# Performance work log

Hardware: AMD Instinct MI355X
Metric: run time of the kernel (lower is better)

Reference implementation:

```python
import jax, jax.numpy as jnp
import numpy as np

HIDDEN = 32
ODE_H = 0.1      # rk4 fixed step size (torchdiffeq options step_size=0.1)
ODE_STEPS = 10   # integrate t in [0, 1]


def gcn_conv(x, W, b, edge_index, n):
    """PyG GCNConv: symmetric norm with self-loops; x' = D^-1/2 (A+I) D^-1/2 (x W) + b."""
    h = x @ W                                  # [n, out]
    src, dst = edge_index[0], edge_index[1]
    deg = jnp.ones((n,), h.dtype).at[dst].add(1.0)   # +1 for self-loop
    dinv = jax.lax.rsqrt(deg)
    coef = (dinv[src] * dinv[dst])[:, None]
    agg = jnp.zeros_like(h).at[dst].add(h[src] * coef)
    agg = agg + h * (dinv * dinv)[:, None]     # self-loop term
    return agg + b


def ode_rk4(x0, edge_index, Wg, bg, wt, n):
    """RK4 integration of psi(t,x)=relu(GCN(x)) * sigmoid(t * wt) from t=0 to 1."""
    def f(t, x):
        gate = jax.nn.sigmoid(t * wt)          # [hidden], Linear(1,h,no bias).sigmoid()
        return jax.nn.relu(gcn_conv(x, Wg, bg, edge_index, n)) * gate

    h = ODE_H
    def step(x, t):
        k1 = f(t, x)
        k2 = f(t + h * 0.5, x + (h * 0.5) * k1)
        k3 = f(t + h * 0.5, x + (h * 0.5) * k2)
        k4 = f(t + h, x + h * k3)
        return x + (h / 6.0) * (k1 + 2.0 * k2 + 2.0 * k3 + k4), None

    ts = jnp.arange(ODE_STEPS, dtype=x0.dtype) * h
    xf, _ = jax.lax.scan(step, x0, ts)
    return xf


def setup_inputs() -> dict:
    key = jax.random.key(0)
    ks = jax.random.split(key, 16)
    N, IN, H = 100000, 128, HIDDEN
    E, DE = 1600000, 800000

    inp = {
        "H_t": jax.random.normal(ks[0], (N, IN), jnp.float32),
        "A_pos_t": jax.random.randint(ks[1], (2, E), 0, N),
        "A_neg_t": jax.random.randint(ks[2], (2, E), 0, N),
        "dA_pos": jax.random.randint(ks[3], (2, DE), 0, N),
        "dA_neg": jax.random.randint(ks[4], (2, DE), 0, N),
        # init GCN
        "W_init": jax.random.normal(ks[5], (IN, H), jnp.float32) / np.sqrt(IN),
        "b_init": jnp.zeros((H,), jnp.float32),
        # pos ODE func
        "W_pos": jax.random.normal(ks[6], (H, H), jnp.float32) / np.sqrt(H),
        "b_pos": jnp.zeros((H,), jnp.float32),
        "wt_pos": jax.random.normal(ks[7], (H,), jnp.float32),
        # neg ODE func
        "W_neg": jax.random.normal(ks[8], (H, H), jnp.float32) / np.sqrt(H),
        "b_neg": jnp.zeros((H,), jnp.float32),
        "wt_neg": jax.random.normal(ks[9], (H,), jnp.float32),
        # combine + layernorm
        "W_comb": jax.random.normal(ks[10], (2 * H, H), jnp.float32) / np.sqrt(2 * H),
        "b_comb": jnp.zeros((H,), jnp.float32),
        "ln_g": jnp.ones((H,), jnp.float32),
        "ln_b": jnp.zeros((H,), jnp.float32),
    }
    return inp


def reference(H_t, A_pos_t, A_neg_t, dA_pos, dA_neg,
              W_init, b_init, W_pos, b_pos, wt_pos,
              W_neg, b_neg, wt_neg, W_comb, b_comb, ln_g, ln_b):
    n = H_t.shape[0]
    edges_all = jnp.concatenate([A_pos_t, A_neg_t], axis=1)
    H = jax.nn.relu(gcn_conv(H_t, W_init, b_init, edges_all, n))   # [n, hidden]
    Z_pos = ode_rk4(H, dA_pos, W_pos, b_pos, wt_pos, n)
    Z_neg = ode_rk4(H, dA_neg, W_neg, b_neg, wt_neg, n)
    Z = jnp.concatenate([Z_pos, Z_neg], axis=-1) @ W_comb + b_comb # [n, hidden]
    mu = jnp.mean(Z, axis=-1, keepdims=True)
    var = jnp.var(Z, axis=-1, keepdims=True)
    return (Z - mu) * jax.lax.rsqrt(var + 1e-5) * ln_g + ln_b
```

## Files before the change

### kernel.cpp

```cpp
#include <hip/hip_runtime.h>
#include <math.h>


#define TPB 256
#define SCAN_T 1024

typedef _Float16 h8 __attribute__((ext_vector_type(8)));
typedef float f8 __attribute__((ext_vector_type(8)));


struct SegG { const int* src; const int* dst; int n; int goff; };
struct FSeg { const int* src; const int* dst; int n; const int* offs; int* cur; };

__global__ void count4(SegG s0, SegG s1, SegG s2, SegG s3, int* __restrict__ cnt3,
                       int* __restrict__ rank) {
    int i = blockIdx.x * blockDim.x + threadIdx.x;
    SegG s; int e;
    if (i < s0.n) { s = s0; e = i; }
    else if (i < s0.n + s1.n) { s = s1; e = i - s0.n; }
    else if (i < s0.n + s1.n + s2.n) { s = s2; e = i - s0.n - s1.n; }
    else if (i < s0.n + s1.n + s2.n + s3.n) { s = s3; e = i - s0.n - s1.n - s2.n; }
    else return;
    int r = atomicAdd(&cnt3[s.goff + s.dst[e]], 1);
    if (rank) rank[i] = r;
}

__global__ void fill4_rank(SegG s0, SegG s1, SegG s2, SegG s3,
                           const int* __restrict__ offs3, const int* __restrict__ rank,
                           int* __restrict__ csr) {
    int i = blockIdx.x * blockDim.x + threadIdx.x;
    SegG s; int e;
    if (i < s0.n) { s = s0; e = i; }
    else if (i < s0.n + s1.n) { s = s1; e = i - s0.n; }
    else if (i < s0.n + s1.n + s2.n) { s = s2; e = i - s0.n - s1.n; }
    else if (i < s0.n + s1.n + s2.n + s3.n) { s = s3; e = i - s0.n - s1.n - s2.n; }
    else return;
    csr[offs3[s.goff + s.dst[e]] + rank[i]] = s.src[e];
}

__global__ void fill4(FSeg s0, FSeg s1, FSeg s2, FSeg s3, int* __restrict__ csr) {
    int i = blockIdx.x * blockDim.x + threadIdx.x;
    FSeg s; int e;
    if (i < s0.n) { s = s0; e = i; }
    else if (i < s0.n + s1.n) { s = s1; e = i - s0.n; }
    else if (i < s0.n + s1.n + s2.n) { s = s2; e = i - s0.n - s1.n; }
    else if (i < s0.n + s1.n + s2.n + s3.n) { s = s3; e = i - s0.n - s1.n - s2.n; }
    else return;
    int d = s.dst[e];
    int pos = s.offs[d] + atomicAdd(&s.cur[d], 1);
    csr[pos] = s.src[e];
}

__global__ void dinv_from_cnt(const int* __restrict__ cnt, float* __restrict__ dinv, int n) {
    int i = blockIdx.x * blockDim.x + threadIdx.x;
    if (i < n) dinv[i] = rsqrtf(1.0f + (float)cnt[i]);
}

__global__ void scan_block(const int* __restrict__ in, int n, int* __restrict__ out,
                           int* __restrict__ bsums) {
    __shared__ int sh[SCAN_T];
    int tx = threadIdx.x;
    int g = blockIdx.x * SCAN_T + tx;
    int v = (g < n) ? in[g] : 0;
    sh[tx] = v;
    __syncthreads();
    for (int off = 1; off < SCAN_T; off <<= 1) {
        int t = (tx >= off) ? sh[tx - off] : 0;
        __syncthreads();
        sh[tx] += t;
        __syncthreads();
    }
    if (g < n) out[g] = sh[tx] - v;
    if (tx == SCAN_T - 1) bsums[blockIdx.x] = sh[tx];
}

__global__ void scan_sums(int* __restrict__ bsums, int nb) {
    __shared__ int sh[SCAN_T];
    int tx = threadIdx.x;
    int v = (tx < nb) ? bsums[tx] : 0;
    sh[tx] = v;
    __syncthreads();
    for (int off = 1; off < SCAN_T; off <<= 1) {
        int t = (tx >= off) ? sh[tx - off] : 0;
        __syncthreads();
        sh[tx] += t;
        __syncthreads();
    }
    if (tx < nb) bsums[tx] = sh[tx] - v;
}

__global__ void scan_add(int* __restrict__ offs, const int* __restrict__ bsums, int n, int total) {
    int g = blockIdx.x * blockDim.x + threadIdx.x;
    if (g < n) offs[g] += bsums[g >> 10];
    if (g == 0) offs[n] = total;
}


__global__ void mm32_kernel(const float* __restrict__ x, const float* __restrict__ W,
                            const float* __restrict__ dinv, _Float16* __restrict__ hs, int N) {
    __shared__ float Ws[32][32];
    __shared__ float xs[8][32];
    int tid = threadIdx.x;
    for (int i = tid; i < 32 * 32; i += TPB) Ws[i >> 5][i & 31] = W[i];
    int base = blockIdx.x * 8;
    {
        int idx = base * 32 + tid;
        xs[tid >> 5][tid & 31] = (idx < N * 32) ? x[idx] : 0.0f;
    }
    __syncthreads();
    int row = tid >> 5, c = tid & 31;
    int gr = base + row;
    float acc = 0.0f;
#pragma unroll
    for (int k = 0; k < 32; ++k) acc += xs[row][k] * Ws[k][c];
    if (gr < N) hs[gr * 32 + c] = (_Float16)(acc * dinv[gr]);
}

__global__ void mm128_kernel(const float* __restrict__ x, const float* __restrict__ W,
                             const float* __restrict__ dinv, _Float16* __restrict__ hs, int N) {
    __shared__ float Ws[128][32];
    __shared__ float xs[8][128];
    int tid = threadIdx.x;
    for (int i = tid; i < 128 * 32; i += TPB) Ws[i >> 5][i & 31] = W[i];
    int base = blockIdx.x * 8;
    for (int i = tid; i < 8 * 128; i += TPB) {
        int idx = base * 128 + i;
        xs[i >> 7][i & 127] = (idx < N * 128) ? x[idx] : 0.0f;
    }
    __syncthreads();
    int row = tid >> 5, c = tid & 31;
    int gr = base + row;
    float acc = 0.0f;
#pragma unroll
    for (int k = 0; k < 128; ++k) acc += xs[row][k] * Ws[k][c];
    if (gr < N) hs[gr * 32 + c] = (_Float16)(acc * dinv[gr]);
}


struct Job {
    const int* offs; const int* csr;
    const _Float16* hs_in; _Float16* hs_out;
    const float* dinv; const float* dinv_next;
    const float* bias; const float* wt;
    _Float16* ksum; float* x;
    const float* W;
};

__global__ __launch_bounds__(TPB) void agg_stage(Job jp, Job jn, int nbg, float t,
                                                 int stage, int do_mm, int split,
                                                 float* __restrict__ x2, int N) {
    __shared__ float Ws[32][32];
    __shared__ float xts[64][36];
    __shared__ int soffs[65];

    bool isP; int bid;
    if (split) {
        int xcd = blockIdx.x & 7;
        isP = xcd < 4;
        bid = ((int)blockIdx.x >> 3) * 4 + (xcd & 3);
        if (bid >= nbg) return;
    } else {
        isP = (int)blockIdx.x < nbg;
        bid = isP ? blockIdx.x : (blockIdx.x - nbg);
    }
    const Job& J = isP ? jp : jn;
    int nbase = bid * 64;
    int tid = threadIdx.x;
    int lnode = tid >> 2, q = tid & 3;
    int node = nbase + lnode;
    bool valid = node < N;

    if (do_mm) {
        for (int i = tid; i < 32 * 32; i += TPB) Ws[i >> 5][i & 31] = J.W[i];
    }
    if (tid < 65) {
        int ix = nbase + tid; if (ix > N) ix = N;
        soffs[tid] = J.offs[ix];
    }
    __syncthreads();

    f8 xrow;
#pragma unroll
    for (int j = 0; j < 8; ++j) xrow[j] = 0.f;

    if (valid) {
        const h8* hsv = (const h8*)J.hs_in;
        const int* __restrict__ csr = J.csr;
        int r0 = soffs[lnode], r1 = soffs[lnode + 1];
        f8 acc = __builtin_convertvector(hsv[node * 4 + q], f8);
        int i = r0;
        for (; i + 4 <= r1; i += 4) {
            int s0 = csr[i], s1 = csr[i + 1], s2 = csr[i + 2], s3 = csr[i + 3];
            h8 v0 = hsv[s0 * 4 + q];
            h8 v1 = hsv[s1 * 4 + q];
            h8 v2 = hsv[s2 * 4 + q];
            h8 v3 = hsv[s3 * 4 + q];
            acc += (__builtin_convertvector(v0, f8) + __builtin_convertvector(v1, f8))
                 + (__builtin_convertvector(v2, f8) + __builtin_convertvector(v3, f8));
        }
        for (; i < r1; ++i)
            acc += __builtin_convertvector(hsv[csr[i] * 4 + q], f8);

        float dv = J.dinv[node];
        f8 bb = ((const f8*)J.bias)[q];
        f8 kv;
#pragma unroll
        for (int j = 0; j < 8; ++j) kv[j] = fmaxf(acc[j] * dv + bb[j], 0.f);
        if (J.wt) {
            f8 w = ((const f8*)J.wt)[q];
#pragma unroll
            for (int j = 0; j < 8; ++j) kv[j] *= 1.f / (1.f + expf(-t * w[j]));
        }
        int idx = node * 4 + q;
        f8* x8 = (f8*)J.x;
        h8* ks8 = (h8*)J.ksum;
        if (stage == 0) {
            x8[idx] = kv;
            ((f8*)x2)[idx] = kv;
            xrow = kv;
        } else if (stage == 4) {
            f8 ks = __builtin_convertvector(ks8[idx], f8);
            f8 xv = x8[idx];
            const float cc = 0.1f / 6.0f;
#pragma unroll
            for (int j = 0; j < 8; ++j) xv[j] += cc * (ks[j] + kv[j]);
            x8[idx] = xv;
            xrow = xv;
        } else {
            float a = (stage == 3) ? 0.1f : 0.05f;
            f8 xv = x8[idx];
#pragma unroll
            for (int j = 0; j < 8; ++j) xrow[j] = xv[j] + a * kv[j];
            if (stage == 1) {
                ks8[idx] = __builtin_convertvector(kv, h8);
            } else {
                f8 ks = __builtin_convertvector(ks8[idx], f8);
#pragma unroll
                for (int j = 0; j < 8; ++j) ks[j] += 2.f * kv[j];
                ks8[idx] = __builtin_convertvector(ks, h8);
            }
        }
    }

    if (do_mm) {
        if (valid) {
#pragma unroll
            for (int j = 0; j < 8; ++j) xts[lnode][q * 8 + j] = xrow[j];
        }
        __syncthreads();
        if (valid) {
            f8 accm;
#pragma unroll
            for (int j = 0; j < 8; ++j) accm[j] = 0.f;
#pragma unroll
            for (int k = 0; k < 32; ++k) {
                float xv = xts[lnode][k];
                f8 w = *(const f8*)&Ws[k][q * 8];
                accm += xv * w;
            }
            accm *= J.dinv_next[node];
            ((h8*)J.hs_out)[node * 4 + q] = __builtin_convertvector(accm, h8);
        }
    }
}


__global__ void combine_kernel(const float* __restrict__ zp, const float* __restrict__ zn,
                               const float* __restrict__ Wc, const float* __restrict__ bc,
                               const float* __restrict__ g, const float* __restrict__ be,
                               float* __restrict__ out, int N) {
    __shared__ float Ws[64][32];
    __shared__ float zs[8][64];
    int tid = threadIdx.x;
    for (int i = tid; i < 64 * 32; i += TPB) Ws[i >> 5][i & 31] = Wc[i];
    int base = blockIdx.x * 8;
    {
        int r = tid >> 5, c = tid & 31;
        int gr = base + r;
        zs[r][c] = (gr < N) ? zp[gr * 32 + c] : 0.0f;
        zs[r][32 + c] = (gr < N) ? zn[gr * 32 + c] : 0.0f;
    }
    __syncthreads();
    int row = tid >> 5, c = tid & 31;
    int gr = base + row;
    float acc = bc[c];
#pragma unroll
    for (int k = 0; k < 64; ++k) acc += zs[row][k] * Ws[k][c];
    float s = acc, sq = acc * acc;
#pragma unroll
    for (int off = 16; off; off >>= 1) {
        s += __shfl_xor(s, off, 32);
        sq += __shfl_xor(sq, off, 32);
    }
    float mu = s * (1.0f / 32.0f);
    float var = sq * (1.0f / 32.0f) - mu * mu;
    float y = (acc - mu) * rsqrtf(var + 1e-5f) * g[c] + be[c];
    if (gr < N) out[gr * 32 + c] = y;
}


extern "C" void kernel_launch(void* const* d_in, const int* in_sizes, int n_in,
                              void* d_out, int out_size, void* d_ws, size_t ws_size,
                              hipStream_t stream) {
    const float* H_t = (const float*)d_in[0];
    const int* Apos = (const int*)d_in[1];
    const int* Aneg = (const int*)d_in[2];
    const int* dApos = (const int*)d_in[3];
    const int* dAneg = (const int*)d_in[4];
    const float* W_init = (const float*)d_in[5];
    const float* b_init = (const float*)d_in[6];
    const float* W_pos = (const float*)d_in[7];
    const float* b_pos = (const float*)d_in[8];
    const float* wt_pos = (const float*)d_in[9];
    const float* W_neg = (const float*)d_in[10];
    const float* b_neg = (const float*)d_in[11];
    const float* wt_neg = (const float*)d_in[12];
    const float* W_comb = (const float*)d_in[13];
    const float* b_comb = (const float*)d_in[14];
    const float* ln_g = (const float*)d_in[15];
    const float* ln_b = (const float*)d_in[16];

    const int N = in_sizes[0] / 128;
    const int E1 = in_sizes[1] / 2;
    const int E2 = in_sizes[2] / 2;
    const int DE1 = in_sizes[3] / 2;
    const int DE2 = in_sizes[4] / 2;
    const int Etot = E1 + E2 + DE1 + DE2;

    const int* Apos_src = Apos, * Apos_dst = Apos + E1;
    const int* Aneg_src = Aneg, * Aneg_dst = Aneg + E2;
    const int* dApos_src = dApos, * dApos_dst = dApos + DE1;
    const int* dAneg_src = dAneg, * dAneg_dst = dAneg + DE2;

    const size_t n32 = (size_t)N * 32;
    const size_t szf = n32 * 4;
    const size_t szh = n32 * 2;
    auto al = [](size_t b) { return (b + 255) & ~(size_t)255; };

    size_t small_bytes = 3 * al((size_t)(3 * N) * 4)
                       + al((3 * (size_t)N + 1) * 4)
                       + al((size_t)Etot * 4)
                       + al(SCAN_T * 4);
    size_t need_merged = 2 * al(szf) + 6 * al(szh) + small_bytes;
    size_t need_rank = need_merged + al((size_t)Etot * 4);
    bool merged = ws_size >= need_merged + 4096;
    bool use_rank = ws_size >= need_rank + 4096;

    char* p = (char*)d_ws;
    auto alloc = [&](size_t bytes) -> void* {
        void* r = (void*)p;
        p += al(bytes);
        return r;
    };
    float* x_pos = (float*)alloc(szf);
    float* x_neg = (float*)alloc(szf);
    _Float16* ksum_p = (_Float16*)alloc(szh);
    _Float16* ksum_n = merged ? (_Float16*)alloc(szh) : ksum_p;
    _Float16* hs_pa = (_Float16*)alloc(szh);
    _Float16* hs_pb = (_Float16*)alloc(szh);
    _Float16* hs_na = merged ? (_Float16*)alloc(szh) : hs_pa;
    _Float16* hs_nb = merged ? (_Float16*)alloc(szh) : hs_pb;
    float* dinv3 = (float*)alloc((size_t)(3 * N) * 4);
    int* cnt3 = (int*)alloc((size_t)(3 * N) * 4);
    int* cur3 = (int*)alloc((size_t)(3 * N) * 4);
    int* offs3 = (int*)alloc((3 * (size_t)N + 1) * 4);
    int* csr3 = (int*)alloc((size_t)Etot * 4);
    int* bsums = (int*)alloc(SCAN_T * 4);
    int* rank = use_rank ? (int*)alloc((size_t)Etot * 4) : nullptr;

    size_t used = (size_t)(p - (char*)d_ws);
    if (used > ws_size) used = ws_size;

    hipMemsetAsync(d_ws, 0, used, stream);

    float* dinv_all = dinv3, * dinv_pos = dinv3 + N, * dinv_neg = dinv3 + 2 * N;
    const int* offs_all = offs3, * offs_pos = offs3 + N, * offs_neg = offs3 + 2 * N;

    dim3 blk(TPB);
    auto gblk = [](int n) { return dim3((n + TPB - 1) / TPB); };
    dim3 grid_rows((N + 7) / 8);
    const int nb64 = (N + 63) / 64;
    const int n3 = 3 * N;
    const int nbs = (n3 + SCAN_T - 1) / SCAN_T;
    const int nsplit = ((nb64 + 3) / 4) * 8;

    SegG s0 = { Apos_src, Apos_dst, E1, 0 };
    SegG s1 = { Aneg_src, Aneg_dst, E2, 0 };
    SegG s2 = { dApos_src, dApos_dst, DE1, N };
    SegG s3 = { dAneg_src, dAneg_dst, DE2, 2 * N };
    count4<<<gblk(Etot), blk, 0, stream>>>(s0, s1, s2, s3, cnt3, rank);
    dinv_from_cnt<<<gblk(n3), blk, 0, stream>>>(cnt3, dinv3, n3);
    scan_block<<<nbs, SCAN_T, 0, stream>>>(cnt3, n3, offs3, bsums);
    scan_sums<<<1, SCAN_T, 0, stream>>>(bsums, nbs);
    scan_add<<<gblk(n3), blk, 0, stream>>>(offs3, bsums, n3, Etot);
    if (use_rank) {
        fill4_rank<<<gblk(Etot), blk, 0, stream>>>(s0, s1, s2, s3, offs3, rank, csr3);
    } else {
        FSeg f0 = { Apos_src, Apos_dst, E1, offs3, cur3 };
        FSeg f1 = { Aneg_src, Aneg_dst, E2, offs3, cur3 };
        FSeg f2 = { dApos_src, dApos_dst, DE1, offs3 + N, cur3 + N };
        FSeg f3 = { dAneg_src, dAneg_dst, DE2, offs3 + 2 * N, cur3 + 2 * N };
        fill4<<<gblk(Etot), blk, 0, stream>>>(f0, f1, f2, f3, csr3);
    }

    auto mkjob = [&](const int* offs, const _Float16* hs_in, _Float16* hs_out,
                     const float* dinv, const float* dinv_next, const float* bias,
                     const float* wt, _Float16* ksum, float* x, const float* W) {
        Job j; j.offs = offs; j.csr = csr3; j.hs_in = hs_in; j.hs_out = hs_out;
        j.dinv = dinv; j.dinv_next = dinv_next; j.bias = bias; j.wt = wt;
        j.ksum = ksum; j.x = x; j.W = W; return j;
    };

    mm128_kernel<<<grid_rows, blk, 0, stream>>>(H_t, W_init, dinv_all, hs_pa, N);
    {
        Job j0 = mkjob(offs_all, hs_pa, hs_pb, dinv_all, dinv_pos, b_init,
                       nullptr, nullptr, x_pos, W_pos);
        agg_stage<<<nb64, blk, 0, stream>>>(j0, j0, nb64, 0.0f, 0, 1, 0, x_neg, N);
    }

    if (merged) {
        mm32_kernel<<<grid_rows, blk, 0, stream>>>(x_neg, W_neg, dinv_neg, hs_nb, N);
        for (int s = 0; s < 10; ++s) {
            float t0 = 0.1f * (float)s;
            int last_mm = (s == 9) ? 0 : 1;
            Job p1 = mkjob(offs_pos, hs_pb, hs_pa, dinv_pos, dinv_pos, b_pos, wt_pos, ksum_p, x_pos, W_pos);
            Job n1 = mkjob(offs_neg, hs_nb, hs_na, dinv_neg, dinv_neg, b_neg, wt_neg, ksum_n, x_neg, W_neg);
            agg_stage<<<nsplit, blk, 0, stream>>>(p1, n1, nb64, t0, 1, 1, 1, nullptr, N);
            Job p2 = p1; p2.hs_in = hs_pa; p2.hs_out = hs_pb;
            Job n2 = n1; n2.hs_in = hs_na; n2.hs_out = hs_nb;
            agg_stage<<<nsplit, blk, 0, stream>>>(p2, n2, nb64, t0 + 0.05f, 2, 1, 1, nullptr, N);
            agg_stage<<<nsplit, blk, 0, stream>>>(p1, n1, nb64, t0 + 0.05f, 3, 1, 1, nullptr, N);
            agg_stage<<<nsplit, blk, 0, stream>>>(p2, n2, nb64, t0 + 0.1f, 4, last_mm, 1, nullptr, N);
        }
    } else {
        for (int ode = 0; ode < 2; ++ode) {
            float* x = ode ? x_neg : x_pos;
            const float* W = ode ? W_neg : W_pos;
            const float* b = ode ? b_neg : b_pos;
            const float* wt = ode ? wt_neg : wt_pos;
            const float* dinv = ode ? dinv_neg : dinv_pos;
            const int* offs = ode ? offs_neg : offs_pos;
            if (ode == 1) {
                mm32_kernel<<<grid_rows, blk, 0, stream>>>(x, W, dinv, hs_pb, N);
            }
            for (int s = 0; s < 10; ++s) {
                float t0 = 0.1f * (float)s;
                int last_mm = (s == 9) ? 0 : 1;
                Job j1 = mkjob(offs, hs_pb, hs_pa, dinv, dinv, b, wt, ksum_p, x, W);
                Job j2 = j1; j2.hs_in = hs_pa; j2.hs_out = hs_pb;
                agg_stage<<<nb64, blk, 0, stream>>>(j1, j1, nb64, t0, 1, 1, 0, nullptr, N);
                agg_stage<<<nb64, blk, 0, stream>>>(j2, j2, nb64, t0 + 0.05f, 2, 1, 0, nullptr, N);
                agg_stage<<<nb64, blk, 0, stream>>>(j1, j1, nb64, t0 + 0.05f, 3, 1, 0, nullptr, N);
                agg_stage<<<nb64, blk, 0, stream>>>(j2, j2, nb64, t0 + 0.1f, 4, last_mm, 0, nullptr, N);
            }
        }
    }

    combine_kernel<<<grid_rows, blk, 0, stream>>>(x_pos, x_neg, W_comb, b_comb, ln_g, ln_b,
                                                  (float*)d_out, N);
}
```

Baseline: 2.043 ms.

## Replicate CSR degree counters per XCD to localize histogram atomics

Keeps eight copies of the per-node degree counters, one per XCD, chosen by reading the hardware XCC_ID register. Each edge does its atomic increment on its own die's copy with workgroup scope, which avoids atomics bouncing across dies. A merge kernel sums the copies and computes dinv, and a fused scan pass turns them into per-XCD base offsets for the fill step. The cost is eight times the counter memory, extra merge traffic, and a reliance on workgroup-scope atomics staying coherent within an XCD's L2.

```diff
diff --git a/kernel.cpp b/kernel.cpp
--- a/kernel.cpp
+++ b/kernel.cpp
@@ -7,6 +7,12 @@
 
 typedef _Float16 h8 __attribute__((ext_vector_type(8)));
 typedef float f8 __attribute__((ext_vector_type(8)));
+
+__device__ __forceinline__ int xcc_id() {
+    unsigned v;
+    asm volatile("s_getreg_b32 %0, hwreg(HW_REG_XCC_ID, 0, 4)" : "=s"(v));
+    return (int)(v & 7u);
+}
 
 
 struct SegG { const int* src; const int* dst; int n; int goff; };
@@ -25,6 +31,32 @@
     if (rank) rank[i] = r;
 }
 
+__global__ void count4_xcd(SegG s0, SegG s1, SegG s2, SegG s3,
+                           int* __restrict__ rep, int n3, int* __restrict__ rank) {
+    int i = blockIdx.x * blockDim.x + threadIdx.x;
+    SegG s; int e;
+    if (i < s0.n) { s = s0; e = i; }
+    else if (i < s0.n + s1.n) { s = s1; e = i - s0.n; }
+    else if (i < s0.n + s1.n + s2.n) { s = s2; e = i - s0.n - s1.n; }
+    else if (i < s0.n + s1.n + s2.n + s3.n) { s = s3; e = i - s0.n - s1.n - s2.n; }
+    else return;
+    int xcd = xcc_id();
+    int r = __hip_atomic_fetch_add(&rep[xcd * n3 + s.goff + s.dst[e]], 1,
+                                   __ATOMIC_RELAXED, __HIP_MEMORY_SCOPE_WORKGROUP);
+    rank[i] = (xcd << 28) | r;
+}
+
+__global__ void merge_cnt(const int* __restrict__ rep, int n3,
+                          int* __restrict__ cnt, float* __restrict__ dinv) {
+    int i = blockIdx.x * blockDim.x + threadIdx.x;
+    if (i >= n3) return;
+    int c = 0;
+#pragma unroll
+    for (int x = 0; x < 8; ++x) c += rep[x * n3 + i];
+    cnt[i] = c;
+    dinv[i] = rsqrtf(1.0f + (float)c);
+}
+
 __global__ void fill4_rank(SegG s0, SegG s1, SegG s2, SegG s3,
                            const int* __restrict__ offs3, const int* __restrict__ rank,
                            int* __restrict__ csr) {
@@ -36,6 +68,22 @@
     else if (i < s0.n + s1.n + s2.n + s3.n) { s = s3; e = i - s0.n - s1.n - s2.n; }
     else return;
     csr[offs3[s.goff + s.dst[e]] + rank[i]] = s.src[e];
+}
+
+__global__ void fill4_rank_xcd(SegG s0, SegG s1, SegG s2, SegG s3,
+                               const int* __restrict__ rep, int n3,
+                               const int* __restrict__ rank, int* __restrict__ csr) {
+    int i = blockIdx.x * blockDim.x + threadIdx.x;
+    SegG s; int e;
+    if (i < s0.n) { s = s0; e = i; }
+    else if (i < s0.n + s1.n) { s = s1; e = i - s0.n; }
+    else if (i < s0.n + s1.n + s2.n) { s = s2; e = i - s0.n - s1.n; }
+    else if (i < s0.n + s1.n + s2.n + s3.n) { s = s3; e = i - s0.n - s1.n - s2.n; }
+    else return;
+    unsigned rv = (unsigned)rank[i];
+    int x = (int)(rv >> 28);
+    int lr = (int)(rv & 0x0FFFFFFFu);
+    csr[rep[x * n3 + s.goff + s.dst[e]] + lr] = s.src[e];
 }
 
 __global__ void fill4(FSeg s0, FSeg s1, FSeg s2, FSeg s3, int* __restrict__ csr) {
@@ -92,6 +140,23 @@
 __global__ void scan_add(int* __restrict__ offs, const int* __restrict__ bsums, int n, int total) {
     int g = blockIdx.x * blockDim.x + threadIdx.x;
     if (g < n) offs[g] += bsums[g >> 10];
+    if (g == 0) offs[n] = total;
+}
+
+__global__ void scan_add_fuse(int* __restrict__ offs, const int* __restrict__ bsums,
+                              int n, int total, int* __restrict__ rep) {
+    int g = blockIdx.x * blockDim.x + threadIdx.x;
+    if (g < n) {
+        int off = offs[g] + bsums[g >> 10];
+        offs[g] = off;
+        int run = off;
+#pragma unroll
+        for (int x = 0; x < 8; ++x) {
+            int t = rep[x * n + g];
+            rep[x * n + g] = run;
+            run += t;
+        }
+    }
     if (g == 0) offs[n] = total;
 }
 
@@ -326,6 +391,7 @@
     const int DE1 = in_sizes[3] / 2;
     const int DE2 = in_sizes[4] / 2;
     const int Etot = E1 + E2 + DE1 + DE2;
+    const int n3 = 3 * N;
 
     const int* Apos_src = Apos, * Apos_dst = Apos + E1;
     const int* Aneg_src = Aneg, * Aneg_dst = Aneg + E2;
@@ -337,14 +403,16 @@
     const size_t szh = n32 * 2;
     auto al = [](size_t b) { return (b + 255) & ~(size_t)255; };
 
-    size_t small_bytes = 3 * al((size_t)(3 * N) * 4)
-                       + al((3 * (size_t)N + 1) * 4)
+    size_t small_bytes = 3 * al((size_t)n3 * 4)
+                       + al(((size_t)n3 + 1) * 4)
                        + al((size_t)Etot * 4)
                        + al(SCAN_T * 4);
     size_t need_merged = 2 * al(szf) + 6 * al(szh) + small_bytes;
     size_t need_rank = need_merged + al((size_t)Etot * 4);
+    size_t need_xcd = need_rank + al((size_t)8 * n3 * 4);
     bool merged = ws_size >= need_merged + 4096;
     bool use_rank = ws_size >= need_rank + 4096;
+    bool use_xcd = ws_size >= need_xcd + 4096;
 
     char* p = (char*)d_ws;
     auto alloc = [&](size_t bytes) -> void* {
@@ -360,13 +428,14 @@
     _Float16* hs_pb = (_Float16*)alloc(szh);
     _Float16* hs_na = merged ? (_Float16*)alloc(szh) : hs_pa;
     _Float16* hs_nb = merged ? (_Float16*)alloc(szh) : hs_pb;
-    float* dinv3 = (float*)alloc((size_t)(3 * N) * 4);
-    int* cnt3 = (int*)alloc((size_t)(3 * N) * 4);
-    int* cur3 = (int*)alloc((size_t)(3 * N) * 4);
-    int* offs3 = (int*)alloc((3 * (size_t)N + 1) * 4);
+    float* dinv3 = (float*)alloc((size_t)n3 * 4);
+    int* cnt3 = (int*)alloc((size_t)n3 * 4);
+    int* cur3 = (int*)alloc((size_t)n3 * 4);
+    int* offs3 = (int*)alloc(((size_t)n3 + 1) * 4);
     int* csr3 = (int*)alloc((size_t)Etot * 4);
     int* bsums = (int*)alloc(SCAN_T * 4);
     int* rank = use_rank ? (int*)alloc((size_t)Etot * 4) : nullptr;
+    int* rep = use_xcd ? (int*)alloc((size_t)8 * n3 * 4) : nullptr;
 
     size_t used = (size_t)(p - (char*)d_ws);
     if (used > ws_size) used = ws_size;
@@ -380,7 +449,6 @@
     auto gblk = [](int n) { return dim3((n + TPB - 1) / TPB); };
     dim3 grid_rows((N + 7) / 8);
     const int nb64 = (N + 63) / 64;
-    const int n3 = 3 * N;
     const int nbs = (n3 + SCAN_T - 1) / SCAN_T;
     const int nsplit = ((nb64 + 3) / 4) * 8;
 
@@ -388,19 +456,28 @@
     SegG s1 = { Aneg_src, Aneg_dst, E2, 0 };
     SegG s2 = { dApos_src, dApos_dst, DE1, N };
     SegG s3 = { dAneg_src, dAneg_dst, DE2, 2 * N };
-    count4<<<gblk(Etot), blk, 0, stream>>>(s0, s1, s2, s3, cnt3, rank);
-    dinv_from_cnt<<<gblk(n3), blk, 0, stream>>>(cnt3, dinv3, n3);
-    scan_block<<<nbs, SCAN_T, 0, stream>>>(cnt3, n3, offs3, bsums);
-    scan_sums<<<1, SCAN_T, 0, stream>>>(bsums, nbs);
-    scan_add<<<gblk(n3), blk, 0, stream>>>(offs3, bsums, n3, Etot);
-    if (use_rank) {
-        fill4_rank<<<gblk(Etot), blk, 0, stream>>>(s0, s1, s2, s3, offs3, rank, csr3);
+    if (use_xcd) {
+        count4_xcd<<<gblk(Etot), blk, 0, stream>>>(s0, s1, s2, s3, rep, n3, rank);
+        merge_cnt<<<gblk(n3), blk, 0, stream>>>(rep, n3, cnt3, dinv3);
+        scan_block<<<nbs, SCAN_T, 0, stream>>>(cnt3, n3, offs3, bsums);
+        scan_sums<<<1, SCAN_T, 0, stream>>>(bsums, nbs);
+        scan_add_fuse<<<gblk(n3), blk, 0, stream>>>(offs3, bsums, n3, Etot, rep);
+        fill4_rank_xcd<<<gblk(Etot), blk, 0, stream>>>(s0, s1, s2, s3, rep, n3, rank, csr3);
     } else {
-        FSeg f0 = { Apos_src, Apos_dst, E1, offs3, cur3 };
-        FSeg f1 = { Aneg_src, Aneg_dst, E2, offs3, cur3 };
-        FSeg f2 = { dApos_src, dApos_dst, DE1, offs3 + N, cur3 + N };
-        FSeg f3 = { dAneg_src, dAneg_dst, DE2, offs3 + 2 * N, cur3 + 2 * N };
-        fill4<<<gblk(Etot), blk, 0, stream>>>(f0, f1, f2, f3, csr3);
+        count4<<<gblk(Etot), blk, 0, stream>>>(s0, s1, s2, s3, cnt3, rank);
+        dinv_from_cnt<<<gblk(n3), blk, 0, stream>>>(cnt3, dinv3, n3);
+        scan_block<<<nbs, SCAN_T, 0, stream>>>(cnt3, n3, offs3, bsums);
+        scan_sums<<<1, SCAN_T, 0, stream>>>(bsums, nbs);
+        scan_add<<<gblk(n3), blk, 0, stream>>>(offs3, bsums, n3, Etot);
+        if (use_rank) {
+            fill4_rank<<<gblk(Etot), blk, 0, stream>>>(s0, s1, s2, s3, offs3, rank, csr3);
+        } else {
+            FSeg f0 = { Apos_src, Apos_dst, E1, offs3, cur3 };
+            FSeg f1 = { Aneg_src, Aneg_dst, E2, offs3, cur3 };
+            FSeg f2 = { dApos_src, dApos_dst, DE1, offs3 + N, cur3 + N };
+            FSeg f3 = { dAneg_src, dAneg_dst, DE2, offs3 + 2 * N, cur3 + 2 * N };
+            fill4<<<gblk(Etot), blk, 0, stream>>>(f0, f1, f2, f3, csr3);
+        }
     }
 
     auto mkjob = [&](const int* offs, const _Float16* hs_in, _Float16* hs_out,
```

Result: no change. 2.032 ms (-0.6%).

## Fuse edge counting with input projection and fold degree scaling into gather

Applied to the files above, without the earlier changes.

Merges the edge-count atomics and the 128->32 input matmul into one interleaved launch, so the matmul no longer needs dinv and instead applies source-side dinv during the first aggregation gather. Computes dinv inside the scan kernel, drops the separate dinv and mm128 launches, stores per-edge ranks as 16-bit values and narrows the workspace memset to the counters. This cuts launches and memory traffic in the graph-build phase, at the cost of extra per-edge dinv loads in the initial gather and an assumption that in-degrees fit in 16 bits.

```diff
diff --git a/kernel.cpp b/kernel.cpp
--- a/kernel.cpp
+++ b/kernel.cpp
@@ -12,21 +12,50 @@
 struct SegG { const int* src; const int* dst; int n; int goff; };
 struct FSeg { const int* src; const int* dst; int n; const int* offs; int* cur; };
 
-__global__ void count4(SegG s0, SegG s1, SegG s2, SegG s3, int* __restrict__ cnt3,
-                       int* __restrict__ rank) {
-    int i = blockIdx.x * blockDim.x + threadIdx.x;
-    SegG s; int e;
-    if (i < s0.n) { s = s0; e = i; }
-    else if (i < s0.n + s1.n) { s = s1; e = i - s0.n; }
-    else if (i < s0.n + s1.n + s2.n) { s = s2; e = i - s0.n - s1.n; }
-    else if (i < s0.n + s1.n + s2.n + s3.n) { s = s3; e = i - s0.n - s1.n - s2.n; }
-    else return;
-    int r = atomicAdd(&cnt3[s.goff + s.dst[e]], 1);
-    if (rank) rank[i] = r;
+__global__ __launch_bounds__(TPB) void count_mm(
+        SegG s0, SegG s1, SegG s2, SegG s3, int* __restrict__ cnt3,
+        unsigned short* __restrict__ rank,
+        const float* __restrict__ x, const float* __restrict__ W,
+        _Float16* __restrict__ hs, int N, int cntB, int mmB) {
+    __shared__ float Ws[128][32];
+    __shared__ float xs[8][128];
+
+    int g5 = blockIdx.x / 5, r5 = blockIdx.x % 5;
+    if (r5 < 3) {
+        int cb = g5 * 3 + r5;
+        if (cb >= cntB) return;
+        int i = cb * TPB + threadIdx.x;
+        SegG s; int e;
+        if (i < s0.n) { s = s0; e = i; }
+        else if (i < s0.n + s1.n) { s = s1; e = i - s0.n; }
+        else if (i < s0.n + s1.n + s2.n) { s = s2; e = i - s0.n - s1.n; }
+        else if (i < s0.n + s1.n + s2.n + s3.n) { s = s3; e = i - s0.n - s1.n - s2.n; }
+        else return;
+        int r = atomicAdd(&cnt3[s.goff + s.dst[e]], 1);
+        if (rank) rank[i] = (unsigned short)r;
+    } else {
+        int mb = g5 * 2 + (r5 - 3);
+        if (mb >= mmB) return;
+        int tid = threadIdx.x;
+        for (int i = tid; i < 128 * 32; i += TPB) Ws[i >> 5][i & 31] = W[i];
+        int base = mb * 8;
+        for (int i = tid; i < 8 * 128; i += TPB) {
+            int idx = base * 128 + i;
+            xs[i >> 7][i & 127] = (idx < N * 128) ? x[idx] : 0.0f;
+        }
+        __syncthreads();
+        int row = tid >> 5, c = tid & 31;
+        int gr = base + row;
+        float acc = 0.0f;
+#pragma unroll
+        for (int k = 0; k < 128; ++k) acc += xs[row][k] * Ws[k][c];
+        if (gr < N) hs[gr * 32 + c] = (_Float16)acc;
+    }
 }
 
 __global__ void fill4_rank(SegG s0, SegG s1, SegG s2, SegG s3,
-                           const int* __restrict__ offs3, const int* __restrict__ rank,
+                           const int* __restrict__ offs3,
+                           const unsigned short* __restrict__ rank,
                            int* __restrict__ csr) {
     int i = blockIdx.x * blockDim.x + threadIdx.x;
     SegG s; int e;
@@ -35,7 +64,7 @@
     else if (i < s0.n + s1.n + s2.n) { s = s2; e = i - s0.n - s1.n; }
     else if (i < s0.n + s1.n + s2.n + s3.n) { s = s3; e = i - s0.n - s1.n - s2.n; }
     else return;
-    csr[offs3[s.goff + s.dst[e]] + rank[i]] = s.src[e];
+    csr[offs3[s.goff + s.dst[e]] + (int)rank[i]] = s.src[e];
 }
 
 __global__ void fill4(FSeg s0, FSeg s1, FSeg s2, FSeg s3, int* __restrict__ csr) {
@@ -51,17 +80,13 @@
     csr[pos] = s.src[e];
 }
 
-__global__ void dinv_from_cnt(const int* __restrict__ cnt, float* __restrict__ dinv, int n) {
-    int i = blockIdx.x * blockDim.x + threadIdx.x;
-    if (i < n) dinv[i] = rsqrtf(1.0f + (float)cnt[i]);
-}
-
 __global__ void scan_block(const int* __restrict__ in, int n, int* __restrict__ out,
-                           int* __restrict__ bsums) {
+                           int* __restrict__ bsums, float* __restrict__ dinv) {
     __shared__ int sh[SCAN_T];
     int tx = threadIdx.x;
     int g = blockIdx.x * SCAN_T + tx;
     int v = (g < n) ? in[g] : 0;
+    if (g < n) dinv[g] = rsqrtf(1.0f + (float)v);
     sh[tx] = v;
     __syncthreads();
     for (int off = 1; off < SCAN_T; off <<= 1) {
@@ -116,26 +141,6 @@
     if (gr < N) hs[gr * 32 + c] = (_Float16)(acc * dinv[gr]);
 }
 
-__global__ void mm128_kernel(const float* __restrict__ x, const float* __restrict__ W,
-                             const float* __restrict__ dinv, _Float16* __restrict__ hs, int N) {
-    __shared__ float Ws[128][32];
-    __shared__ float xs[8][128];
-    int tid = threadIdx.x;
-    for (int i = tid; i < 128 * 32; i += TPB) Ws[i >> 5][i & 31] = W[i];
-    int base = blockIdx.x * 8;
-    for (int i = tid; i < 8 * 128; i += TPB) {
-        int idx = base * 128 + i;
-        xs[i >> 7][i & 127] = (idx < N * 128) ? x[idx] : 0.0f;
-    }
-    __syncthreads();
-    int row = tid >> 5, c = tid & 31;
-    int gr = base + row;
-    float acc = 0.0f;
-#pragma unroll
-    for (int k = 0; k < 128; ++k) acc += xs[row][k] * Ws[k][c];
-    if (gr < N) hs[gr * 32 + c] = (_Float16)(acc * dinv[gr]);
-}
-
 
 struct Job {
     const int* offs; const int* csr;
@@ -144,6 +149,7 @@
     const float* bias; const float* wt;
     _Float16* ksum; float* x;
     const float* W;
+    const float* sdinv;
 };
 
 __global__ __launch_bounds__(TPB) void agg_stage(Job jp, Job jn, int nbg, float t,
@@ -187,19 +193,42 @@
         const h8* hsv = (const h8*)J.hs_in;
         const int* __restrict__ csr = J.csr;
         int r0 = soffs[lnode], r1 = soffs[lnode + 1];
-        f8 acc = __builtin_convertvector(hsv[node * 4 + q], f8);
-        int i = r0;
-        for (; i + 4 <= r1; i += 4) {
-            int s0 = csr[i], s1 = csr[i + 1], s2 = csr[i + 2], s3 = csr[i + 3];
-            h8 v0 = hsv[s0 * 4 + q];
-            h8 v1 = hsv[s1 * 4 + q];
-            h8 v2 = hsv[s2 * 4 + q];
-            h8 v3 = hsv[s3 * 4 + q];
-            acc += (__builtin_convertvector(v0, f8) + __builtin_convertvector(v1, f8))
-                 + (__builtin_convertvector(v2, f8) + __builtin_convertvector(v3, f8));
-        }
-        for (; i < r1; ++i)
-            acc += __builtin_convertvector(hsv[csr[i] * 4 + q], f8);
+        f8 acc;
+        if (J.sdinv) {
+            const float* __restrict__ sd = J.sdinv;
+            acc = __builtin_convertvector(hsv[node * 4 + q], f8) * sd[node];
+            int i = r0;
+            for (; i + 4 <= r1; i += 4) {
+                int e0 = csr[i], e1 = csr[i + 1], e2 = csr[i + 2], e3 = csr[i + 3];
+                float d0 = sd[e0], d1 = sd[e1], d2 = sd[e2], d3 = sd[e3];
+                h8 v0 = hsv[e0 * 4 + q];
+                h8 v1 = hsv[e1 * 4 + q];
+                h8 v2 = hsv[e2 * 4 + q];
+                h8 v3 = hsv[e3 * 4 + q];
+                acc += __builtin_convertvector(v0, f8) * d0
+                     + __builtin_convertvector(v1, f8) * d1
+                     + __builtin_convertvector(v2, f8) * d2
+                     + __builtin_convertvector(v3, f8) * d3;
+            }
+            for (; i < r1; ++i) {
+                int e = csr[i];
+                acc += __builtin_convertvector(hsv[e * 4 + q], f8) * sd[e];
+            }
+        } else {
+            acc = __builtin_convertvector(hsv[node * 4 + q], f8);
+            int i = r0;
+            for (; i + 4 <= r1; i += 4) {
+                int e0 = csr[i], e1 = csr[i + 1], e2 = csr[i + 2], e3 = csr[i + 3];
+                h8 v0 = hsv[e0 * 4 + q];
+                h8 v1 = hsv[e1 * 4 + q];
+                h8 v2 = hsv[e2 * 4 + q];
+                h8 v3 = hsv[e3 * 4 + q];
+                acc += (__builtin_convertvector(v0, f8) + __builtin_convertvector(v1, f8))
+                     + (__builtin_convertvector(v2, f8) + __builtin_convertvector(v3, f8));
+            }
+            for (; i < r1; ++i)
+                acc += __builtin_convertvector(hsv[csr[i] * 4 + q], f8);
+        }
 
         float dv = J.dinv[node];
         f8 bb = ((const f8*)J.bias)[q];
@@ -326,6 +355,7 @@
     const int DE1 = in_sizes[3] / 2;
     const int DE2 = in_sizes[4] / 2;
     const int Etot = E1 + E2 + DE1 + DE2;
+    const int n3 = 3 * N;
 
     const int* Apos_src = Apos, * Apos_dst = Apos + E1;
     const int* Aneg_src = Aneg, * Aneg_dst = Aneg + E2;
@@ -337,12 +367,12 @@
     const size_t szh = n32 * 2;
     auto al = [](size_t b) { return (b + 255) & ~(size_t)255; };
 
-    size_t small_bytes = 3 * al((size_t)(3 * N) * 4)
-                       + al((3 * (size_t)N + 1) * 4)
+    size_t small_bytes = 3 * al((size_t)n3 * 4)
+                       + al(((size_t)n3 + 1) * 4)
                        + al((size_t)Etot * 4)
                        + al(SCAN_T * 4);
     size_t need_merged = 2 * al(szf) + 6 * al(szh) + small_bytes;
-    size_t need_rank = need_merged + al((size_t)Etot * 4);
+    size_t need_rank = need_merged + al((size_t)Etot * 2);
     bool merged = ws_size >= need_merged + 4096;
     bool use_rank = ws_size >= need_rank + 4096;
 
@@ -360,18 +390,15 @@
     _Float16* hs_pb = (_Float16*)alloc(szh);
     _Float16* hs_na = merged ? (_Float16*)alloc(szh) : hs_pa;
     _Float16* hs_nb = merged ? (_Float16*)alloc(szh) : hs_pb;
-    float* dinv3 = (float*)alloc((size_t)(3 * N) * 4);
-    int* cnt3 = (int*)alloc((size_t)(3 * N) * 4);
-    int* cur3 = (int*)alloc((size_t)(3 * N) * 4);
-    int* offs3 = (int*)alloc((3 * (size_t)N + 1) * 4);
+    float* dinv3 = (float*)alloc((size_t)n3 * 4);
+    int* cnt3 = (int*)alloc((size_t)n3 * 4);
+    int* cur3 = (int*)alloc((size_t)n3 * 4);
+    int* offs3 = (int*)alloc(((size_t)n3 + 1) * 4);
     int* csr3 = (int*)alloc((size_t)Etot * 4);
     int* bsums = (int*)alloc(SCAN_T * 4);
-    int* rank = use_rank ? (int*)alloc((size_t)Etot * 4) : nullptr;
-
-    size_t used = (size_t)(p - (char*)d_ws);
-    if (used > ws_size) used = ws_size;
-
-    hipMemsetAsync(d_ws, 0, used, stream);
+    unsigned short* rank = use_rank ? (unsigned short*)alloc((size_t)Etot * 2) : nullptr;
+
+    hipMemsetAsync(cnt3, 0, 2 * al((size_t)n3 * 4), stream);
 
     float* dinv_all = dinv3, * dinv_pos = dinv3 + N, * dinv_neg = dinv3 + 2 * N;
     const int* offs_all = offs3, * offs_pos = offs3 + N, * offs_neg = offs3 + 2 * N;
@@ -380,7 +407,6 @@
     auto gblk = [](int n) { return dim3((n + TPB - 1) / TPB); };
     dim3 grid_rows((N + 7) / 8);
     const int nb64 = (N + 63) / 64;
-    const int n3 = 3 * N;
     const int nbs = (n3 + SCAN_T - 1) / SCAN_T;
     const int nsplit = ((nb64 + 3) / 4) * 8;
 
@@ -388,9 +414,14 @@
     SegG s1 = { Aneg_src, Aneg_dst, E2, 0 };
     SegG s2 = { dApos_src, dApos_dst, DE1, N };
     SegG s3 = { dAneg_src, dAneg_dst, DE2, 2 * N };
-    count4<<<gblk(Etot), blk, 0, stream>>>(s0, s1, s2, s3, cnt3, rank);
-    dinv_from_cnt<<<gblk(n3), blk, 0, stream>>>(cnt3, dinv3, n3);
-    scan_block<<<nbs, SCAN_T, 0, stream>>>(cnt3, n3, offs3, bsums);
+    {
+        const int cntB = (Etot + TPB - 1) / TPB;
+        const int mmB = (N + 7) / 8;
+        const int g5 = max((cntB + 2) / 3, (mmB + 1) / 2);
+        count_mm<<<dim3(5 * g5), blk, 0, stream>>>(s0, s1, s2, s3, cnt3, rank,
+                                                   H_t, W_init, hs_pa, N, cntB, mmB);
+    }
+    scan_block<<<nbs, SCAN_T, 0, stream>>>(cnt3, n3, offs3, bsums, dinv3);
     scan_sums<<<1, SCAN_T, 0, stream>>>(bsums, nbs);
     scan_add<<<gblk(n3), blk, 0, stream>>>(offs3, bsums, n3, Etot);
     if (use_rank) {
@@ -405,16 +436,16 @@
 
     auto mkjob = [&](const int* offs, const _Float16* hs_in, _Float16* hs_out,
                      const float* dinv, const float* dinv_next, const float* bias,
-                     const float* wt, _Float16* ksum, float* x, const float* W) {
+                     const float* wt, _Float16* ksum, float* x, const float* W,
+                     const float* sdinv) {
         Job j; j.offs = offs; j.csr = csr3; j.hs_in = hs_in; j.hs_out = hs_out;
         j.dinv = dinv; j.dinv_next = dinv_next; j.bias = bias; j.wt = wt;
-        j.ksum = ksum; j.x = x; j.W = W; return j;
+        j.ksum = ksum; j.x = x; j.W = W; j.sdinv = sdinv; return j;
     };
 
-    mm128_kernel<<<grid_rows, blk, 0, stream>>>(H_t, W_init, dinv_all, hs_pa, N);
     {
         Job j0 = mkjob(offs_all, hs_pa, hs_pb, dinv_all, dinv_pos, b_init,
-                       nullptr, nullptr, x_pos, W_pos);
+                       nullptr, nullptr, x_pos, W_pos, dinv_all);
         agg_stage<<<nb64, blk, 0, stream>>>(j0, j0, nb64, 0.0f, 0, 1, 0, x_neg, N);
     }
 
@@ -423,8 +454,8 @@
         for (int s = 0; s < 10; ++s) {
             float t0 = 0.1f * (float)s;
             int last_mm = (s == 9) ? 0 : 1;
-            Job p1 = mkjob(offs_pos, hs_pb, hs_pa, dinv_pos, dinv_pos, b_pos, wt_pos, ksum_p, x_pos, W_pos);
-            Job n1 = mkjob(offs_neg, hs_nb, hs_na, dinv_neg, dinv_neg, b_neg, wt_neg, ksum_n, x_neg, W_neg);
+            Job p1 = mkjob(offs_pos, hs_pb, hs_pa, dinv_pos, dinv_pos, b_pos, wt_pos, ksum_p, x_pos, W_pos, nullptr);
+            Job n1 = mkjob(offs_neg, hs_nb, hs_na, dinv_neg, dinv_neg, b_neg, wt_neg, ksum_n, x_neg, W_neg, nullptr);
             agg_stage<<<nsplit, blk, 0, stream>>>(p1, n1, nb64, t0, 1, 1, 1, nullptr, N);
             Job p2 = p1; p2.hs_in = hs_pa; p2.hs_out = hs_pb;
             Job n2 = n1; n2.hs_in = hs_na; n2.hs_out = hs_nb;
@@ -446,7 +477,7 @@
             for (int s = 0; s < 10; ++s) {
                 float t0 = 0.1f * (float)s;
                 int last_mm = (s == 9) ? 0 : 1;
-                Job j1 = mkjob(offs, hs_pb, hs_pa, dinv, dinv, b, wt, ksum_p, x, W);
+                Job j1 = mkjob(offs, hs_pb, hs_pa, dinv, dinv, b, wt, ksum_p, x, W, nullptr);
                 Job j2 = j1; j2.hs_in = hs_pa; j2.hs_out = hs_pb;
                 agg_stage<<<nb64, blk, 0, stream>>>(j1, j1, nb64, t0, 1, 1, 0, nullptr, N);
                 agg_stage<<<nb64, blk, 0, stream>>>(j2, j2, nb64, t0 + 0.05f, 2, 1, 0, nullptr, N);
```

New measurement: 2.023 ms. No clear change (-1.0%).
